# Kernel tuning notes

Measured on AMD Instinct MI355X. Metric: run time of the kernel, lower is better.

The kernel has to match this reference:

```python
import jax, jax.numpy as jnp
import numpy as np
from jax import lax

M1, M2 = 16, 16  # retained Fourier modes per spatial dim


def _spectral_conv(x, w1, w2):
    # x: [B, C, H, W] real; w1/w2: [C, C, M1, M2, 2] (re, im)
    B, C, H, W = x.shape
    xf = jnp.fft.rfft2(x, norm='ortho')            # [B, C, H, W//2+1] complex
    w1c = w1[..., 0] + 1j * w1[..., 1]
    w2c = w2[..., 0] + 1j * w2[..., 1]
    top = jnp.einsum('bixy,ioxy->boxy', xf[:, :, :M1, :M2], w1c)
    bot = jnp.einsum('bixy,ioxy->boxy', xf[:, :, -M1:, :M2], w2c)
    of = jnp.zeros((B, C, H, W // 2 + 1), dtype=xf.dtype)
    of = of.at[:, :, :M1, :M2].set(top).at[:, :, -M1:, :M2].set(bot)
    return jnp.fft.irfft2(of, s=(H, W), norm='ortho')


def _fno_block(x, w1, w2, skip_w):
    # spectral conv + linear (1x1 conv, no bias) skip
    return _spectral_conv(x, w1, w2) + jnp.einsum('bixy,io->boxy', x, skip_w)


def setup_inputs() -> dict:
    key = jax.random.key(0)
    ks = jax.random.split(key, 6)
    B, T, C, H, W = 4, 8, 64, 64, 64
    scale = 1.0 / (C * C)
    return {
        'x': jax.random.normal(ks[0], (B, T, C, H, W), dtype=jnp.float32),
        'sw1': jax.random.normal(ks[1], (6, C, C, M1, M2, 2), dtype=jnp.float32) * scale,
        'sw2': jax.random.normal(ks[2], (6, C, C, M1, M2, 2), dtype=jnp.float32) * scale,
        'skw': jax.random.normal(ks[3], (6, C, C), dtype=jnp.float32) * 0.02,
        'gate_b': jax.random.normal(ks[4], (3,), dtype=jnp.float32),
        'bias_h': jax.random.normal(ks[5], (1,), dtype=jnp.float32),
    }


def reference(x, sw1, sw2, skw, gate_b, bias_h):
    B, T, C, H, W = x.shape

    def f(i, inp):
        return _fno_block(inp, sw1[i], sw2[i], skw[i])

    def cell(xt, h):
        z = jax.nn.sigmoid(f(0, xt) + f(1, h) + gate_b[0])
        r = jax.nn.sigmoid(f(2, xt) + f(3, h) + gate_b[1])
        h_hat = jax.nn.selu(f(4, xt) + f(5, r * h) + gate_b[2])
        return (1.0 - z) * h + z * h_hat

    def step(h, xt):
        h = cell(xt, h)
        return h, None

    h0 = jnp.full((B, C, H, W), bias_h[0], dtype=x.dtype)
    h_final, _ = lax.scan(step, h0, jnp.moveaxis(x, 1, 0))  # scan over T
    return h_final  # return_sequences=False -> final hidden state [B, C, H, W]
```

## Files before the change

### kernel.cpp

```cpp
#include <hip/hip_runtime.h>

#define BB_ 4
#define TT_ 8
#define CC_ 64
#define HW 4096
#define UMAP 1024
#define STEP 0.09817477042468103f

#define OFF_UXALL 0
#define OFF_UH    (OFF_UXALL + TT_*256*UMAP)
#define OFF_URH   (OFF_UH + 256*UMAP)
#define OFF_SX    (OFF_URH + 256*UMAP)
#define OFF_SPART (OFF_SX + 3*TT_*256*UMAP)
#define OFF_H     (OFF_SPART + 2*8*256*UMAP)
#define OFF_Z     (OFF_H + BB_*CC_*HW)
#define OFF_RH    (OFF_Z + BB_*CC_*HW)
#define OFF_PH    (OFF_RH + BB_*CC_*HW)

__global__ __launch_bounds__(256) void k_init(float* __restrict__ hb,
                                              float* __restrict__ Uh,
                                              const float* __restrict__ bias_h) {
    float v = bias_h[0];
    int blk = blockIdx.x;
    if (blk < 1024) {
        int idx = (blk * 256 + threadIdx.x) * 4;
        *(float4*)(hb + idx) = make_float4(v, v, v, v);
    } else {
        int map = blk - 1024;
        float4 z = make_float4(0.f, 0.f, 0.f, 0.f);
        if (threadIdx.x == 0) z.x = 64.f * v;
        *(float4*)(Uh + (size_t)map * UMAP + threadIdx.x * 4) = z;
    }
}

__device__ __forceinline__ void dft_stages(const float* __restrict__ su,
                                           float* __restrict__ FxR, float* __restrict__ FxI,
                                           float* __restrict__ dst) {
    int tid = threadIdx.x;
    int kx = tid & 15, yb = tid >> 4;
    float stc, sts;
    __sincosf(-STEP * (float)kx, &sts, &stc);
    float wr = 1.f, wi = 0.f;
    float aR[4] = {0, 0, 0, 0}, aI[4] = {0, 0, 0, 0};
    for (int x = 0; x < 64; x++) {
        #pragma unroll
        for (int j = 0; j < 4; j++) {
            float v = su[(yb + 16 * j) * 65 + x];
            aR[j] = fmaf(v, wr, aR[j]);
            aI[j] = fmaf(v, wi, aI[j]);
        }
        float t = wr * stc - wi * sts;
        wi = wr * sts + wi * stc;
        wr = t;
    }
    #pragma unroll
    for (int j = 0; j < 4; j++) {
        FxR[(yb + 16 * j) * 16 + kx] = aR[j];
        FxI[(yb + 16 * j) * 16 + kx] = aI[j];
    }
    __syncthreads();
    int kb = tid >> 4;
    float c0, s0, c1, s1;
    __sincosf(-STEP * (float)kb, &s0, &c0);
    __sincosf(-STEP * (float)(kb + 48), &s1, &c1);
    float w0r = 1, w0i = 0, w1r = 1, w1i = 0;
    float A0r = 0, A0i = 0, A1r = 0, A1i = 0;
    for (int y = 0; y < 64; y++) {
        float Fr = FxR[y * 16 + kx], Fi = FxI[y * 16 + kx];
        A0r = fmaf(Fr, w0r, A0r); A0r = fmaf(-Fi, w0i, A0r);
        A0i = fmaf(Fr, w0i, A0i); A0i = fmaf(Fi, w0r, A0i);
        A1r = fmaf(Fr, w1r, A1r); A1r = fmaf(-Fi, w1i, A1r);
        A1i = fmaf(Fr, w1i, A1i); A1i = fmaf(Fi, w1r, A1i);
        float t0 = w0r * c0 - w0i * s0; w0i = w0r * s0 + w0i * c0; w0r = t0;
        float t1 = w1r * c1 - w1i * s1; w1i = w1r * s1 + w1i * c1; w1r = t1;
    }
    const float sc = 1.f / 64.f;
    float2* d2 = (float2*)dst;
    d2[kb * 16 + kx]        = make_float2(A0r * sc, A0i * sc);
    d2[(kb + 16) * 16 + kx] = make_float2(A1r * sc, A1i * sc);
}

__global__ __launch_bounds__(256) void k_dft_x(const float* __restrict__ x,
                                               float* __restrict__ Uxall) {
    __shared__ float su[64 * 65];
    __shared__ float FxR[1024], FxI[1024];
    int blk = blockIdx.x;
    int t = blk >> 8, map = blk & 255;
    int b = map >> 6, c = map & 63;
    const float* src = x + (((size_t)b * TT_ + t) * CC_ + c) * HW;
    int tid = threadIdx.x;
    #pragma unroll
    for (int k = 0; k < 4; k++) {
        int off = k * 1024 + tid * 4;
        float4 v = *(const float4*)(src + off);
        int y = off >> 6, xx = off & 63;
        su[y * 65 + xx + 0] = v.x; su[y * 65 + xx + 1] = v.y;
        su[y * 65 + xx + 2] = v.z; su[y * 65 + xx + 3] = v.w;
    }
    __syncthreads();
    dft_stages(su, FxR, FxI, Uxall + ((size_t)t * 256 + map) * UMAP);
}

__device__ __forceinline__ void mix_load(const float2* __restrict__ W2,
                                         const float2* __restrict__ U2, int i,
                                         float2 w[4], float2 u[4]) {
    const float2* wp = W2 + (size_t)i * 16384;
    const float2* up = U2 + (size_t)i * 512;
    w[0] = wp[0]; w[1] = wp[256]; w[2] = wp[512]; w[3] = wp[768];
    u[0] = up[0]; u[1] = up[32768]; u[2] = up[65536]; u[3] = up[98304];
}

__device__ __forceinline__ void mix_fma(const float2 w[4], const float2 u[4],
                                        float aR[4][4], float aI[4][4]) {
    #pragma unroll
    for (int oo = 0; oo < 4; oo++)
        #pragma unroll
        for (int bb = 0; bb < 4; bb++) {
            aR[oo][bb] = fmaf(u[bb].x, w[oo].x, aR[oo][bb]);
            aR[oo][bb] = fmaf(-u[bb].y, w[oo].y, aR[oo][bb]);
            aI[oo][bb] = fmaf(u[bb].x, w[oo].y, aI[oo][bb]);
            aI[oo][bb] = fmaf(u[bb].y, w[oo].x, aI[oo][bb]);
        }
}

__device__ __forceinline__ void mix_accum(const float2* __restrict__ W2,
                                          const float2* __restrict__ U2,
                                          int niter, float aR[4][4], float aI[4][4])
{
    float2 wA[4], uA[4], wB[4], uB[4], wN[4], uN[4];
    mix_load(W2, U2, 0, wA, uA);
    mix_load(W2, U2, 1, wB, uB);
    for (int i = 0; i + 2 < niter; i += 2) {
        mix_load(W2, U2, i + 2, wN, uN);
        mix_fma(wA, uA, aR, aI);
        #pragma unroll
        for (int k = 0; k < 4; k++) { wA[k] = wN[k]; uA[k] = uN[k]; }
        mix_load(W2, U2, i + 3, wN, uN);
        mix_fma(wB, uB, aR, aI);
        #pragma unroll
        for (int k = 0; k < 4; k++) { wB[k] = wN[k]; uB[k] = uN[k]; }
    }
    mix_fma(wA, uA, aR, aI);
    mix_fma(wB, uB, aR, aI);
}

__device__ __forceinline__ void mix_accum4(const float2* __restrict__ W2,
                                           const float2* __restrict__ U2,
                                           float aR[4][4], float aI[4][4])
{
    float2 w0[4], u0[4], w1[4], u1[4], w2[4], u2[4], w3[4], u3[4], wN[4], uN[4];
    mix_load(W2, U2, 0, w0, u0);
    mix_load(W2, U2, 1, w1, u1);
    mix_load(W2, U2, 2, w2, u2);
    mix_load(W2, U2, 3, w3, u3);
    for (int i = 0; i < 60; i += 4) {
        mix_load(W2, U2, i + 4, wN, uN);
        mix_fma(w0, u0, aR, aI);
        #pragma unroll
        for (int k = 0; k < 4; k++) { w0[k] = wN[k]; u0[k] = uN[k]; }
        mix_load(W2, U2, i + 5, wN, uN);
        mix_fma(w1, u1, aR, aI);
        #pragma unroll
        for (int k = 0; k < 4; k++) { w1[k] = wN[k]; u1[k] = uN[k]; }
        mix_load(W2, U2, i + 6, wN, uN);
        mix_fma(w2, u2, aR, aI);
        #pragma unroll
        for (int k = 0; k < 4; k++) { w2[k] = wN[k]; u2[k] = uN[k]; }
        mix_load(W2, U2, i + 7, wN, uN);
        mix_fma(w3, u3, aR, aI);
        #pragma unroll
        for (int k = 0; k < 4; k++) { w3[k] = wN[k]; u3[k] = uN[k]; }
    }
    mix_fma(w0, u0, aR, aI);
    mix_fma(w1, u1, aR, aI);
    mix_fma(w2, u2, aR, aI);
    mix_fma(w3, u3, aR, aI);
}

__global__ __launch_bounds__(256) void k_mix_x(
    const float* __restrict__ Uxall,
    const float* __restrict__ sw1, const float* __restrict__ sw2,
    float* __restrict__ Sx)
{
    int blk = blockIdx.x;
    int og = blk & 15;
    int half = (blk >> 4) & 1;
    int t = (blk >> 5) & 7;
    int li = blk >> 8;
    int l = li * 2;
    int m = threadIdx.x;
    int o0 = og * 4;
    const float2* wt = (const float2*)(half ? sw2 : sw1);
    const float2* W2 = wt + (((size_t)l * 64) * 64 + o0) * 256 + m;
    const float2* U2 = (const float2*)Uxall + ((size_t)t * 256) * 512 + half * 256 + m;
    float aR[4][4], aI[4][4];
    #pragma unroll
    for (int oo = 0; oo < 4; oo++)
        #pragma unroll
        for (int b = 0; b < 4; b++) { aR[oo][b] = 0.f; aI[oo][b] = 0.f; }
    mix_accum4(W2, U2, aR, aI);
    float2* S2 = (float2*)Sx;
    #pragma unroll
    for (int oo = 0; oo < 4; oo++)
        #pragma unroll
        for (int b = 0; b < 4; b++)
            S2[((size_t)(li * 8 + t) * 256 + b * 64 + o0 + oo) * 512 + half * 256 + m]
                = make_float2(aR[oo][b], aI[oo][b]);
}

__device__ __forceinline__ void mix_body_h(int blk, int l0, int l1,
    const float* __restrict__ U,
    const float* __restrict__ sw1, const float* __restrict__ sw2,
    float* __restrict__ Spart)
{
    int og = blk & 15;
    int ic = (blk >> 4) & 7;
    int half = (blk >> 7) & 1;
    int g = (blk >> 8) & 1;
    int m = threadIdx.x;
    int o0 = og * 4, ib = ic * 8;
    int l = g ? l1 : l0;
    const float2* wt = (const float2*)(half ? sw2 : sw1);
    const float2* W2 = wt + (((size_t)l * 64 + ib) * 64 + o0) * 256 + m;
    const float2* U2 = (const float2*)U + (size_t)ib * 512 + half * 256 + m;
    float aR[4][4], aI[4][4];
    #pragma unroll
    for (int oo = 0; oo < 4; oo++)
        #pragma unroll
        for (int b = 0; b < 4; b++) { aR[oo][b] = 0.f; aI[oo][b] = 0.f; }
    mix_accum(W2, U2, 8, aR, aI);
    float2* S2 = (float2*)Spart;
    #pragma unroll
    for (int oo = 0; oo < 4; oo++)
        #pragma unroll
        for (int b = 0; b < 4; b++)
            S2[((size_t)(g * 8 + ic) * 256 + b * 64 + o0 + oo) * 512 + half * 256 + m]
                = make_float2(aR[oo][b], aI[oo][b]);
}

__device__ __forceinline__ void fma16(const float4 w, const float4 u, float acc[4][4]) {
    acc[0][0] = fmaf(u.x, w.x, acc[0][0]); acc[0][1] = fmaf(u.y, w.x, acc[0][1]);
    acc[0][2] = fmaf(u.z, w.x, acc[0][2]); acc[0][3] = fmaf(u.w, w.x, acc[0][3]);
    acc[1][0] = fmaf(u.x, w.y, acc[1][0]); acc[1][1] = fmaf(u.y, w.y, acc[1][1]);
    acc[1][2] = fmaf(u.z, w.y, acc[1][2]); acc[1][3] = fmaf(u.w, w.y, acc[1][3]);
    acc[2][0] = fmaf(u.x, w.z, acc[2][0]); acc[2][1] = fmaf(u.y, w.z, acc[2][1]);
    acc[2][2] = fmaf(u.z, w.z, acc[2][2]); acc[2][3] = fmaf(u.w, w.z, acc[2][3]);
    acc[3][0] = fmaf(u.x, w.w, acc[3][0]); acc[3][1] = fmaf(u.y, w.w, acc[3][1]);
    acc[3][2] = fmaf(u.z, w.w, acc[3][2]); acc[3][3] = fmaf(u.w, w.w, acc[3][3]);
}

__device__ __forceinline__ void skip_gemm(int rr, float* __restrict__ sW,
    const float* __restrict__ uA, long long bsA,
    const float* __restrict__ uB, long long bsB,
    const float* __restrict__ skw, int lA, int lB, float gb,
    float* __restrict__ out)
{
    int pxc = rr & 31, oh = (rr >> 5) & 1, b = rr >> 6;
    int tid = threadIdx.x;
    int ot = tid & 7, pt = tid >> 3;
    #pragma unroll
    for (int n = 0; n < 4; n++) {
        int idx = n * 1024 + tid * 4;
        int k = idx >> 5, oc = idx & 31;
        int p = k >> 6, i = k & 63;
        *(float4*)(sW + idx) =
            *(const float4*)(skw + (p ? lB : lA) * 4096 + i * 64 + oh * 32 + oc);
    }
    __syncthreads();
    float acc[4][4];
    #pragma unroll
    for (int oo = 0; oo < 4; oo++)
        #pragma unroll
        for (int q = 0; q < 4; q++) acc[oo][q] = 0.f;
    const float* pa = uA + (long long)b * bsA + pxc * 128 + pt * 4;
    const float* pb = uB + (long long)b * bsB + pxc * 128 + pt * 4;
    const float4* sW4 = (const float4*)sW;
    #pragma unroll 4
    for (int i = 0; i < 64; i++) {
        float4 ua = *(const float4*)(pa + (size_t)i * HW);
        float4 wa = sW4[i * 8 + ot];
        fma16(wa, ua, acc);
        float4 ub = *(const float4*)(pb + (size_t)i * HW);
        float4 wb = sW4[(64 + i) * 8 + ot];
        fma16(wb, ub, acc);
    }
    float* op = out + ((long long)(b * 64 + oh * 32 + ot * 4)) * HW + pxc * 128 + pt * 4;
    #pragma unroll
    for (int oo = 0; oo < 4; oo++) {
        float4 r = make_float4(acc[oo][0] + gb, acc[oo][1] + gb,
                               acc[oo][2] + gb, acc[oo][3] + gb);
        *(float4*)(op + (size_t)oo * HW) = r;
    }
}

__global__ __launch_bounds__(256) void k_front_zr(
    const float* __restrict__ Uh,
    const float* __restrict__ xt, const float* __restrict__ hb,
    const float* __restrict__ sw1, const float* __restrict__ sw2,
    const float* __restrict__ skw, const float* __restrict__ gate_b,
    float* __restrict__ Spart, float* __restrict__ zb, float* __restrict__ rhb)
{
    __shared__ float smem[4096];
    int blk = blockIdx.x;
    if (blk < 512) {
        mix_body_h(blk, 1, 3, Uh, sw1, sw2, Spart);
    } else {
        int r = blk - 512;
        int g = r >> 8;
        skip_gemm(r & 255, smem,
                  xt, (long long)TT_ * CC_ * HW, hb, (long long)CC_ * HW,
                  skw, g ? 2 : 0, g ? 3 : 1, gate_b[g], g ? rhb : zb);
    }
}

__global__ __launch_bounds__(256) void k_front_h(
    const float* __restrict__ Urh,
    const float* __restrict__ xt, const float* __restrict__ rhb,
    const float* __restrict__ sw1, const float* __restrict__ sw2,
    const float* __restrict__ skw, const float* __restrict__ gate_b,
    float* __restrict__ Spart, float* __restrict__ phb)
{
    __shared__ float smem[4096];
    int blk = blockIdx.x;
    if (blk < 256) {
        mix_body_h(blk, 5, 5, Urh, sw1, sw2, Spart);
    } else {
        int r = blk - 256;
        skip_gemm(r, smem,
                  xt, (long long)TT_ * CC_ * HW, rhb, (long long)CC_ * HW,
                  skw, 4, 5, gate_b[2], phb);
    }
}

__device__ __forceinline__ void idft_stage1(const float* __restrict__ SR,
                                            const float* __restrict__ SI,
                                            float* __restrict__ GR, float* __restrict__ GI)
{
    int tid = threadIdx.x;
    int kx = tid & 15, yb = tid >> 4;
    #pragma unroll
    for (int j = 0; j < 4; j++) {
        int y = yb + 16 * j;
        float stc, sts;
        __sincosf(STEP * (float)y, &sts, &stc);
        float ar = 0.f, ai = 0.f;
        float wr = 1.f, wi = 0.f;
        for (int k = 0; k < 16; k++) {
            float sr_ = SR[k * 16 + kx], si_ = SI[k * 16 + kx];
            ar = fmaf(sr_, wr, ar); ar = fmaf(-si_, wi, ar);
            ai = fmaf(sr_, wi, ai); ai = fmaf(si_, wr, ai);
            float t = wr * stc - wi * sts; wi = wr * sts + wi * stc; wr = t;
        }
        int q = (3 * y) & 3;
        float w2r = (q == 0) ? 1.f : ((q == 2) ? -1.f : 0.f);
        float w2i = (q == 1) ? 1.f : ((q == 3) ? -1.f : 0.f);
        for (int k = 16; k < 32; k++) {
            float sr_ = SR[k * 16 + kx], si_ = SI[k * 16 + kx];
            ar = fmaf(sr_, w2r, ar); ar = fmaf(-si_, w2i, ar);
            ai = fmaf(sr_, w2i, ai); ai = fmaf(si_, w2r, ai);
            float t = w2r * stc - w2i * sts; w2i = w2r * sts + w2i * stc; w2r = t;
        }
        GR[y * 16 + kx] = ar;
        GI[y * 16 + kx] = ai;
    }
}

__global__ __launch_bounds__(256) void k_back_zr(
    const float* __restrict__ Spart, const float* __restrict__ Sx, int t,
    float* __restrict__ zb, float* __restrict__ rhb,
    const float* __restrict__ hb, float* __restrict__ Urh)
{
    __shared__ float smem[6208];
    float* SR = smem;
    float* SI = smem + 512;
    float* GR = smem + 1024;
    float* GI = smem + 2048;
    int g = blockIdx.x >> 8;
    int map = blockIdx.x & 255;
    int tid = threadIdx.x;
    {
        float4 v = ((const float4*)Sx)[((size_t)(g * 8 + t) * 256 + map) * 256 + tid];
        float sxr = v.x, sxi = v.y, syr = v.z, syi = v.w;
        const float4* base = (const float4*)Spart;
        #pragma unroll
        for (int ic = 0; ic < 8; ic++) {
            float4 p = base[((size_t)(g * 8 + ic) * 256 + map) * 256 + tid];
            sxr += p.x; sxi += p.y; syr += p.z; syi += p.w;
        }
        SR[2 * tid] = sxr; SI[2 * tid] = sxi;
        SR[2 * tid + 1] = syr; SI[2 * tid + 1] = syi;
    }
    __syncthreads();
    idft_stage1(SR, SI, GR, GI);
    __syncthreads();
    int x = tid & 63, ybase = tid >> 6;
    float cx, sx;
    __sincosf(STEP * (float)x, &sx, &cx);
    size_t mo = (size_t)map * HW;
    float rhv[16];
    #pragma unroll
    for (int j = 0; j < 16; j++) {
        int y = ybase + 4 * j;
        float acc = GR[y * 16];
        float wr = cx, wi = sx;
        #pragma unroll
        for (int k = 1; k < 16; k++) {
            acc = fmaf(2.f * GR[y * 16 + k], wr, acc);
            acc = fmaf(-2.f * GI[y * 16 + k], wi, acc);
            float t2 = wr * cx - wi * sx; wi = wr * sx + wi * cx; wr = t2;
        }
        float val = acc * (1.f / 64.f);
        int idx = y * 64 + x;
        if (g == 0) {
            float pre = val + zb[mo + idx];
            zb[mo + idx] = 1.f / (1.f + __expf(-pre));
        } else {
            float pre = val + rhb[mo + idx];
            float rr = 1.f / (1.f + __expf(-pre));
            float rh = rr * hb[mo + idx];
            rhb[mo + idx] = rh;
            rhv[j] = rh;
        }
    }
    if (g == 0) return;
    __syncthreads();
    float* su = smem;
    #pragma unroll
    for (int j = 0; j < 16; j++) {
        int y = ybase + 4 * j;
        su[y * 65 + x] = rhv[j];
    }
    __syncthreads();
    dft_stages(su, smem + 4160, smem + 5184, Urh + (size_t)map * UMAP);
}

__global__ __launch_bounds__(256) void k_back_h(
    const float* __restrict__ Spart, const float* __restrict__ Sx, int t,
    const float* __restrict__ zb, const float* __restrict__ phb,
    float* __restrict__ hb, float* __restrict__ Uh)
{
    __shared__ float smem[6208];
    float* SR = smem;
    float* SI = smem + 512;
    float* GR = smem + 1024;
    float* GI = smem + 2048;
    int map = blockIdx.x & 255;
    int tid = threadIdx.x;
    {
        float4 v = ((const float4*)Sx)[((size_t)(2 * 8 + t) * 256 + map) * 256 + tid];
        float sxr = v.x, sxi = v.y, syr = v.z, syi = v.w;
        const float4* base = (const float4*)Spart;
        #pragma unroll
        for (int ic = 0; ic < 8; ic++) {
            float4 p = base[((size_t)ic * 256 + map) * 256 + tid];
            sxr += p.x; sxi += p.y; syr += p.z; syi += p.w;
        }
        SR[2 * tid] = sxr; SI[2 * tid] = sxi;
        SR[2 * tid + 1] = syr; SI[2 * tid + 1] = syi;
    }
    __syncthreads();
    idft_stage1(SR, SI, GR, GI);
    __syncthreads();
    int x = tid & 63, ybase = tid >> 6;
    float cx, sx;
    __sincosf(STEP * (float)x, &sx, &cx);
    size_t mo = (size_t)map * HW;
    float hv[16];
    #pragma unroll
    for (int j = 0; j < 16; j++) {
        int y = ybase + 4 * j;
        float acc = GR[y * 16];
        float wr = cx, wi = sx;
        #pragma unroll
        for (int k = 1; k < 16; k++) {
            acc = fmaf(2.f * GR[y * 16 + k], wr, acc);
            acc = fmaf(-2.f * GI[y * 16 + k], wi, acc);
            float t2 = wr * cx - wi * sx; wi = wr * sx + wi * cx; wr = t2;
        }
        float val = acc * (1.f / 64.f);
        int idx = y * 64 + x;
        float pre = val + phb[mo + idx];
        float hh = (pre > 0.f) ? 1.0507009873554805f * pre
                               : 1.7580993408473766f * (__expf(pre) - 1.f);
        float z = zb[mo + idx];
        float hn = fmaf(z, hh - hb[mo + idx], hb[mo + idx]);
        hb[mo + idx] = hn;
        hv[j] = hn;
    }
    __syncthreads();
    float* su = smem;
    #pragma unroll
    for (int j = 0; j < 16; j++) {
        int y = ybase + 4 * j;
        su[y * 65 + x] = hv[j];
    }
    __syncthreads();
    dft_stages(su, smem + 4160, smem + 5184, Uh + (size_t)map * UMAP);
}

extern "C" void kernel_launch(void* const* d_in, const int* in_sizes, int n_in,
                              void* d_out, int out_size, void* d_ws, size_t ws_size,
                              hipStream_t stream)
{
    (void)in_sizes; (void)n_in; (void)out_size; (void)ws_size;
    const float* x   = (const float*)d_in[0];
    const float* sw1 = (const float*)d_in[1];
    const float* sw2 = (const float*)d_in[2];
    const float* skw = (const float*)d_in[3];
    const float* gb  = (const float*)d_in[4];
    const float* bh  = (const float*)d_in[5];
    float* ws    = (float*)d_ws;
    float* Uxall = ws + OFF_UXALL;
    float* Uh    = ws + OFF_UH;
    float* Urh   = ws + OFF_URH;
    float* Sx    = ws + OFF_SX;
    float* Sp    = ws + OFF_SPART;
    float* hb    = ws + OFF_H;
    float* zb    = ws + OFF_Z;
    float* rhb   = ws + OFF_RH;
    float* phb   = ws + OFF_PH;

    k_init<<<1280, 256, 0, stream>>>(hb, Uh, bh);
    k_dft_x<<<2048, 256, 0, stream>>>(x, Uxall);
    k_mix_x<<<768, 256, 0, stream>>>(Uxall, sw1, sw2, Sx);
    for (int t = 0; t < TT_; t++) {
        const float* xt = x + (size_t)t * CC_ * HW;
        k_front_zr<<<1024, 256, 0, stream>>>(Uh, xt, hb, sw1, sw2, skw, gb,
                                             Sp, zb, rhb);
        k_back_zr<<<512, 256, 0, stream>>>(Sp, Sx, t, zb, rhb, hb, Urh);
        k_front_h<<<512, 256, 0, stream>>>(Urh, xt, rhb, sw1, sw2, skw, gb,
                                           Sp, phb);
        k_back_h<<<256, 256, 0, stream>>>(Sp, Sx, t, zb, phb, hb, Uh);
    }
    hipMemcpyAsync(d_out, hb, (size_t)BB_ * CC_ * HW * sizeof(float),
                   hipMemcpyDeviceToDevice, stream);
}
```

Measured before the change: 851.8 us.

## Use 512-thread blocks with split-K reduction in mix and inverse-DFT kernels

k_mix_x is restructured into 512-thread blocks that split the 64-channel reduction in two halves, combine the partial sums through shared memory, and re-tile the thread mapping over modes, output groups and time steps. k_back_zr and k_back_h move to 512 threads with one complex value per thread, which halves the per-thread work in the inverse and forward DFT stages. The aim is more in-flight parallelism and shorter per-thread serial chains on the latency-bound recurrent step kernels. The cost is extra shared-memory reduction and synchronisation, plus different register and occupancy behaviour.

Result: faster. 787.2 us (-7.6%).

```diff
diff --git a/kernel.cpp b/kernel.cpp
--- a/kernel.cpp
+++ b/kernel.cpp
@@ -80,6 +80,47 @@
     d2[(kb + 16) * 16 + kx] = make_float2(A1r * sc, A1i * sc);
 }
 
+__device__ __forceinline__ void dft_stages_512(const float* __restrict__ su,
+                                               float* __restrict__ FxR, float* __restrict__ FxI,
+                                               float* __restrict__ dst) {
+    int tid = threadIdx.x;
+    int kx = tid & 15, yb = tid >> 4;
+    float stc, sts;
+    __sincosf(-STEP * (float)kx, &sts, &stc);
+    float wr = 1.f, wi = 0.f;
+    float aR[2] = {0, 0}, aI[2] = {0, 0};
+    for (int x = 0; x < 64; x++) {
+        #pragma unroll
+        for (int j = 0; j < 2; j++) {
+            float v = su[(yb + 32 * j) * 65 + x];
+            aR[j] = fmaf(v, wr, aR[j]);
+            aI[j] = fmaf(v, wi, aI[j]);
+        }
+        float t = wr * stc - wi * sts;
+        wi = wr * sts + wi * stc;
+        wr = t;
+    }
+    #pragma unroll
+    for (int j = 0; j < 2; j++) {
+        FxR[(yb + 32 * j) * 16 + kx] = aR[j];
+        FxI[(yb + 32 * j) * 16 + kx] = aI[j];
+    }
+    __syncthreads();
+    int kb = tid >> 4;
+    int ky = (kb < 16) ? kb : kb + 32;
+    float c0, s0;
+    __sincosf(-STEP * (float)ky, &s0, &c0);
+    float w0r = 1, w0i = 0, A0r = 0, A0i = 0;
+    for (int y = 0; y < 64; y++) {
+        float Fr = FxR[y * 16 + kx], Fi = FxI[y * 16 + kx];
+        A0r = fmaf(Fr, w0r, A0r); A0r = fmaf(-Fi, w0i, A0r);
+        A0i = fmaf(Fr, w0i, A0i); A0i = fmaf(Fi, w0r, A0i);
+        float t0 = w0r * c0 - w0i * s0; w0i = w0r * s0 + w0i * c0; w0r = t0;
+    }
+    const float sc = 1.f / 64.f;
+    ((float2*)dst)[kb * 16 + kx] = make_float2(A0r * sc, A0i * sc);
+}
+
 __global__ __launch_bounds__(256) void k_dft_x(const float* __restrict__ x,
                                                float* __restrict__ Uxall) {
     __shared__ float su[64 * 65];
@@ -144,68 +185,60 @@
     mix_fma(wB, uB, aR, aI);
 }
 
-__device__ __forceinline__ void mix_accum4(const float2* __restrict__ W2,
-                                           const float2* __restrict__ U2,
-                                           float aR[4][4], float aI[4][4])
-{
-    float2 w0[4], u0[4], w1[4], u1[4], w2[4], u2[4], w3[4], u3[4], wN[4], uN[4];
-    mix_load(W2, U2, 0, w0, u0);
-    mix_load(W2, U2, 1, w1, u1);
-    mix_load(W2, U2, 2, w2, u2);
-    mix_load(W2, U2, 3, w3, u3);
-    for (int i = 0; i < 60; i += 4) {
-        mix_load(W2, U2, i + 4, wN, uN);
-        mix_fma(w0, u0, aR, aI);
-        #pragma unroll
-        for (int k = 0; k < 4; k++) { w0[k] = wN[k]; u0[k] = uN[k]; }
-        mix_load(W2, U2, i + 5, wN, uN);
-        mix_fma(w1, u1, aR, aI);
-        #pragma unroll
-        for (int k = 0; k < 4; k++) { w1[k] = wN[k]; u1[k] = uN[k]; }
-        mix_load(W2, U2, i + 6, wN, uN);
-        mix_fma(w2, u2, aR, aI);
-        #pragma unroll
-        for (int k = 0; k < 4; k++) { w2[k] = wN[k]; u2[k] = uN[k]; }
-        mix_load(W2, U2, i + 7, wN, uN);
-        mix_fma(w3, u3, aR, aI);
-        #pragma unroll
-        for (int k = 0; k < 4; k++) { w3[k] = wN[k]; u3[k] = uN[k]; }
-    }
-    mix_fma(w0, u0, aR, aI);
-    mix_fma(w1, u1, aR, aI);
-    mix_fma(w2, u2, aR, aI);
-    mix_fma(w3, u3, aR, aI);
-}
-
-__global__ __launch_bounds__(256) void k_mix_x(
+__global__ __launch_bounds__(512, 4) void k_mix_x(
     const float* __restrict__ Uxall,
     const float* __restrict__ sw1, const float* __restrict__ sw2,
     float* __restrict__ Sx)
 {
+    __shared__ float2 red2[16 * 256];
     int blk = blockIdx.x;
-    int og = blk & 15;
-    int half = (blk >> 4) & 1;
-    int t = (blk >> 5) & 7;
+    int mq = blk & 3;
+    int tp = (blk >> 2) & 3;
+    int op = (blk >> 4) & 7;
+    int half = (blk >> 7) & 1;
     int li = blk >> 8;
     int l = li * 2;
-    int m = threadIdx.x;
-    int o0 = og * 4;
+    int tid = threadIdx.x;
+    int kc = tid >> 8;
+    int r = tid & 255;
+    int ml = r & 15, og1 = (r >> 4) & 1, t1 = (r >> 5) & 1, wq = r >> 6;
+    int m = mq * 64 + wq * 16 + ml;
+    int o0 = (op * 2 + og1) * 4;
+    int t = tp * 2 + t1;
     const float2* wt = (const float2*)(half ? sw2 : sw1);
-    const float2* W2 = wt + (((size_t)l * 64) * 64 + o0) * 256 + m;
-    const float2* U2 = (const float2*)Uxall + ((size_t)t * 256) * 512 + half * 256 + m;
+    const float2* W2 = wt + ((size_t)(l * 4096 + o0)) * 256 + m + (size_t)kc * 32 * 16384;
+    const float2* U2 = (const float2*)Uxall + (size_t)t * 131072 + half * 256 + m
+                       + (size_t)kc * 32 * 512;
     float aR[4][4], aI[4][4];
     #pragma unroll
     for (int oo = 0; oo < 4; oo++)
         #pragma unroll
         for (int b = 0; b < 4; b++) { aR[oo][b] = 0.f; aI[oo][b] = 0.f; }
-    mix_accum4(W2, U2, aR, aI);
-    float2* S2 = (float2*)Sx;
-    #pragma unroll
-    for (int oo = 0; oo < 4; oo++)
-        #pragma unroll
-        for (int b = 0; b < 4; b++)
-            S2[((size_t)(li * 8 + t) * 256 + b * 64 + o0 + oo) * 512 + half * 256 + m]
-                = make_float2(aR[oo][b], aI[oo][b]);
+    #pragma unroll 4
+    for (int i = 0; i < 32; ++i) {
+        float2 w[4], u[4];
+        mix_load(W2, U2, i, w, u);
+        mix_fma(w, u, aR, aI);
+    }
+    if (kc) {
+        #pragma unroll
+        for (int oo = 0; oo < 4; oo++)
+            #pragma unroll
+            for (int b = 0; b < 4; b++)
+                red2[(oo * 4 + b) * 256 + r] = make_float2(aR[oo][b], aI[oo][b]);
+    }
+    __syncthreads();
+    if (kc == 0) {
+        float2* S2 = (float2*)Sx;
+        #pragma unroll
+        for (int oo = 0; oo < 4; oo++)
+            #pragma unroll
+            for (int b = 0; b < 4; b++) {
+                float2 p = red2[(oo * 4 + b) * 256 + r];
+                S2[((size_t)(li * 8 + t) * 256 + b * 64 + o0 + oo) * 512 + half * 256 + m]
+                    = make_float2(aR[oo][b] + p.x, aI[oo][b] + p.y);
+            }
+    }
 }
 
 __device__ __forceinline__ void mix_body_h(int blk, int l0, int l1,
@@ -332,15 +365,15 @@
     }
 }
 
-__device__ __forceinline__ void idft_stage1(const float* __restrict__ SR,
-                                            const float* __restrict__ SI,
-                                            float* __restrict__ GR, float* __restrict__ GI)
+__device__ __forceinline__ void idft_stage1_512(const float* __restrict__ SR,
+                                                const float* __restrict__ SI,
+                                                float* __restrict__ GR, float* __restrict__ GI)
 {
     int tid = threadIdx.x;
     int kx = tid & 15, yb = tid >> 4;
     #pragma unroll
-    for (int j = 0; j < 4; j++) {
-        int y = yb + 16 * j;
+    for (int j = 0; j < 2; j++) {
+        int y = yb + 32 * j;
         float stc, sts;
         __sincosf(STEP * (float)y, &sts, &stc);
         float ar = 0.f, ai = 0.f;
@@ -365,7 +398,7 @@
     }
 }
 
-__global__ __launch_bounds__(256) void k_back_zr(
+__global__ __launch_bounds__(512) void k_back_zr(
     const float* __restrict__ Spart, const float* __restrict__ Sx, int t,
     float* __restrict__ zb, float* __restrict__ rhb,
     const float* __restrict__ hb, float* __restrict__ Urh)
@@ -379,28 +412,27 @@
     int map = blockIdx.x & 255;
     int tid = threadIdx.x;
     {
-        float4 v = ((const float4*)Sx)[((size_t)(g * 8 + t) * 256 + map) * 256 + tid];
-        float sxr = v.x, sxi = v.y, syr = v.z, syi = v.w;
-        const float4* base = (const float4*)Spart;
+        float2 v = ((const float2*)Sx)[((size_t)(g * 8 + t) * 256 + map) * 512 + tid];
+        float sr = v.x, si = v.y;
+        const float2* base = (const float2*)Spart;
         #pragma unroll
         for (int ic = 0; ic < 8; ic++) {
-            float4 p = base[((size_t)(g * 8 + ic) * 256 + map) * 256 + tid];
-            sxr += p.x; sxi += p.y; syr += p.z; syi += p.w;
-        }
-        SR[2 * tid] = sxr; SI[2 * tid] = sxi;
-        SR[2 * tid + 1] = syr; SI[2 * tid + 1] = syi;
-    }
-    __syncthreads();
-    idft_stage1(SR, SI, GR, GI);
+            float2 p = base[((size_t)(g * 8 + ic) * 256 + map) * 512 + tid];
+            sr += p.x; si += p.y;
+        }
+        SR[tid] = sr; SI[tid] = si;
+    }
+    __syncthreads();
+    idft_stage1_512(SR, SI, GR, GI);
     __syncthreads();
     int x = tid & 63, ybase = tid >> 6;
     float cx, sx;
     __sincosf(STEP * (float)x, &sx, &cx);
     size_t mo = (size_t)map * HW;
-    float rhv[16];
-    #pragma unroll
-    for (int j = 0; j < 16; j++) {
-        int y = ybase + 4 * j;
+    float rhv[8];
+    #pragma unroll
+    for (int j = 0; j < 8; j++) {
+        int y = ybase + 8 * j;
         float acc = GR[y * 16];
         float wr = cx, wi = sx;
         #pragma unroll
@@ -426,15 +458,15 @@
     __syncthreads();
     float* su = smem;
     #pragma unroll
-    for (int j = 0; j < 16; j++) {
-        int y = ybase + 4 * j;
+    for (int j = 0; j < 8; j++) {
+        int y = ybase + 8 * j;
         su[y * 65 + x] = rhv[j];
     }
     __syncthreads();
-    dft_stages(su, smem + 4160, smem + 5184, Urh + (size_t)map * UMAP);
-}
-
-__global__ __launch_bounds__(256) void k_back_h(
+    dft_stages_512(su, smem + 4160, smem + 5184, Urh + (size_t)map * UMAP);
+}
+
+__global__ __launch_bounds__(512) void k_back_h(
     const float* __restrict__ Spart, const float* __restrict__ Sx, int t,
     const float* __restrict__ zb, const float* __restrict__ phb,
     float* __restrict__ hb, float* __restrict__ Uh)
@@ -447,28 +479,27 @@
     int map = blockIdx.x & 255;
     int tid = threadIdx.x;
     {
-        float4 v = ((const float4*)Sx)[((size_t)(2 * 8 + t) * 256 + map) * 256 + tid];
-        float sxr = v.x, sxi = v.y, syr = v.z, syi = v.w;
-        const float4* base = (const float4*)Spart;
+        float2 v = ((const float2*)Sx)[((size_t)(2 * 8 + t) * 256 + map) * 512 + tid];
+        float sr = v.x, si = v.y;
+        const float2* base = (const float2*)Spart;
         #pragma unroll
         for (int ic = 0; ic < 8; ic++) {
-            float4 p = base[((size_t)ic * 256 + map) * 256 + tid];
-            sxr += p.x; sxi += p.y; syr += p.z; syi += p.w;
-        }
-        SR[2 * tid] = sxr; SI[2 * tid] = sxi;
-        SR[2 * tid + 1] = syr; SI[2 * tid + 1] = syi;
-    }
-    __syncthreads();
-    idft_stage1(SR, SI, GR, GI);
+            float2 p = base[((size_t)ic * 256 + map) * 512 + tid];
+            sr += p.x; si += p.y;
+        }
+        SR[tid] = sr; SI[tid] = si;
+    }
+    __syncthreads();
+    idft_stage1_512(SR, SI, GR, GI);
     __syncthreads();
     int x = tid & 63, ybase = tid >> 6;
     float cx, sx;
     __sincosf(STEP * (float)x, &sx, &cx);
     size_t mo = (size_t)map * HW;
-    float hv[16];
-    #pragma unroll
-    for (int j = 0; j < 16; j++) {
-        int y = ybase + 4 * j;
+    float hv[8];
+    #pragma unroll
+    for (int j = 0; j < 8; j++) {
+        int y = ybase + 8 * j;
         float acc = GR[y * 16];
         float wr = cx, wi = sx;
         #pragma unroll
@@ -490,12 +521,12 @@
     __syncthreads();
     float* su = smem;
     #pragma unroll
-    for (int j = 0; j < 16; j++) {
-        int y = ybase + 4 * j;
+    for (int j = 0; j < 8; j++) {
+        int y = ybase + 8 * j;
         su[y * 65 + x] = hv[j];
     }
     __syncthreads();
-    dft_stages(su, smem + 4160, smem + 5184, Uh + (size_t)map * UMAP);
+    dft_stages_512(su, smem + 4160, smem + 5184, Uh + (size_t)map * UMAP);
 }
 
 extern "C" void kernel_launch(void* const* d_in, const int* in_sizes, int n_in,
@@ -522,15 +553,15 @@
 
     k_init<<<1280, 256, 0, stream>>>(hb, Uh, bh);
     k_dft_x<<<2048, 256, 0, stream>>>(x, Uxall);
-    k_mix_x<<<768, 256, 0, stream>>>(Uxall, sw1, sw2, Sx);
+    k_mix_x<<<768, 512, 0, stream>>>(Uxall, sw1, sw2, Sx);
     for (int t = 0; t < TT_; t++) {
         const float* xt = x + (size_t)t * CC_ * HW;
         k_front_zr<<<1024, 256, 0, stream>>>(Uh, xt, hb, sw1, sw2, skw, gb,
                                              Sp, zb, rhb);
-        k_back_zr<<<512, 256, 0, stream>>>(Sp, Sx, t, zb, rhb, hb, Urh);
+        k_back_zr<<<512, 512, 0, stream>>>(Sp, Sx, t, zb, rhb, hb, Urh);
         k_front_h<<<512, 256, 0, stream>>>(Urh, xt, rhb, sw1, sw2, skw, gb,
                                            Sp, phb);
-        k_back_h<<<256, 256, 0, stream>>>(Sp, Sx, t, zb, phb, hb, Uh);
+        k_back_h<<<256, 512, 0, stream>>>(Sp, Sx, t, zb, phb, hb, Uh);
     }
     hipMemcpyAsync(d_out, hb, (size_t)BB_ * CC_ * HW * sizeof(float),
                    hipMemcpyDeviceToDevice, stream);
```
